# Performance work log

Measured on AMD Instinct MI355X. Metric: run time of the kernel, lower is better.

## Reference

```python
import jax, jax.numpy as jnp
import numpy as np

ALPHA = 0.05
GDEP = 2


def conv1x1(x, w, b):
    # x: [N,C,V,L], w: [O,C], b: [O]
    return jnp.einsum('ncvl,oc->novl', x, w) + b[None, :, None, None]


def setup_inputs() -> dict:
    key = jax.random.key(0)
    ks = jax.random.split(key, 9)
    N, C, V, L = 32, 32, 400, 12
    c_out = 32
    cat = (GDEP + 1) * C
    s = 0.05
    return {
        'x': jax.random.normal(ks[0], (N, C, V, L), jnp.float32),
        'w_lin1': jax.random.normal(ks[1], (C, C), jnp.float32) * s,
        'b_lin1': jnp.zeros((C,), jnp.float32),
        'w_lin2': jax.random.normal(ks[2], (C, C), jnp.float32) * s,
        'b_lin2': jnp.zeros((C,), jnp.float32),
        'w_mlp1': jax.random.normal(ks[3], (c_out, cat), jnp.float32) * s,
        'b_mlp1': jnp.zeros((c_out,), jnp.float32),
        'w_mlp2': jax.random.normal(ks[4], (c_out, cat), jnp.float32) * s,
        'b_mlp2': jnp.zeros((c_out,), jnp.float32),
    }


def reference(x, w_lin1, b_lin1, w_lin2, b_lin2, w_mlp1, b_mlp1, w_mlp2, b_mlp2):
    # dynamic adjacency: adj[n,v,w,l] = sum_c x1[n,c,v,l] * x2[n,c,w,l]
    x1 = jnp.tanh(conv1x1(x, w_lin1, b_lin1))
    x2 = jnp.tanh(conv1x1(x, w_lin2, b_lin2))
    adj = jnp.einsum('ncvl,ncwl->nvwl', x1, x2)  # [N,V,V,L]
    adj0 = jax.nn.softmax(adj, axis=2)
    adj1 = jax.nn.softmax(jnp.swapaxes(adj, 1, 2), axis=2)

    def diffuse(a):
        h = x
        out = [h]
        for _ in range(GDEP):
            # nconv: h[n,c,w,l] = sum_v h[n,c,v,l] * a[n,v,w,l]
            h = ALPHA * x + (1.0 - ALPHA) * jnp.einsum('ncvl,nvwl->ncwl', h, a)
            out.append(h)
        return jnp.concatenate(out, axis=1)  # [N,(GDEP+1)*C,V,L]

    ho1 = conv1x1(diffuse(adj0), w_mlp1, b_mlp1)
    ho2 = conv1x1(diffuse(adj1), w_mlp2, b_mlp2)
    return ho1 + ho2
```

## Files before the change

### kernel.cpp

```cpp
#include <hip/hip_runtime.h>
#include <stdint.h>

#define TT 1024
#define AL 0.05f
#define OM 0.95f
#define STRD 408
#define LOG2E 1.4426950408889634f

typedef short s4v __attribute__((ext_vector_type(4)));
typedef short s8v __attribute__((ext_vector_type(8)));
typedef float f4v __attribute__((ext_vector_type(4)));
typedef float f16v __attribute__((ext_vector_type(16)));
typedef int   i2v __attribute__((ext_vector_type(2)));

#define MF32(a,b,c) __builtin_amdgcn_mfma_f32_32x32x16_bf16(a,b,c,0,0,0)
#define MF16(a,b,c) __builtin_amdgcn_mfma_f32_16x16x32_bf16(a,b,c,0,0,0)
#define MFP32(a,b,c) __builtin_amdgcn_mfma_f32_32x32x16_fp8_fp8(a,b,c,0,0,0)
#define MFP16(a,b,c) __builtin_amdgcn_mfma_f32_16x16x32_fp8_fp8(a,b,c,0,0,0)

#if __has_builtin(__builtin_amdgcn_exp2f)
#define E2(x) __builtin_amdgcn_exp2f(x)
#else
#define E2(x) exp2f(x)
#endif

__device__ __forceinline__ uint16_t f2bf(float f){ union{float f;uint32_t i;}t; t.f=f; return (uint16_t)((t.i + 0x7fffu + ((t.i>>16)&1u))>>16); }
__device__ __forceinline__ float bf2f(uint16_t h){ union{uint32_t i;float f;}t; t.i=((uint32_t)h)<<16; return t.f; }
__device__ __forceinline__ float bfLO(uint32_t u){ union{uint32_t i;float f;}t; t.i=u<<16; return t.f; }
__device__ __forceinline__ float bfHI(uint32_t u){ union{uint32_t i;float f;}t; t.i=u&0xffff0000u; return t.f; }
__device__ __forceinline__ uint32_t cvtpk(float lo, float hi){ uint32_t r; asm("v_cvt_pk_bf16_f32 %0, %1, %2" : "=v"(r) : "v"(lo), "v"(hi)); return r; }
__device__ __forceinline__ void pl32swap(uint32_t &x, uint32_t &y){
#if __has_builtin(__builtin_amdgcn_permlane32_swap)
  i2v rr = __builtin_amdgcn_permlane32_swap((int)x, (int)y, false, false);
  x = (uint32_t)rr.x; y = (uint32_t)rr.y;
#else
  asm("v_permlane32_swap_b32 %0, %1" : "+v"(x), "+v"(y));
#endif
}
__device__ __forceinline__ float ftanh(float x){ float t = E2(2.885390081777927f*x); return __builtin_fmaf(-2.f, __builtin_amdgcn_rcpf(1.f + t), 1.f); }
__device__ __forceinline__ s8v ld8(const uint16_t* p){ return *(const s8v*)p; }

__device__ __forceinline__ uint32_t sw1fp8(float f){
  union{float f;uint32_t u;}t; t.f=f;
  uint32_t sgn=(t.u>>24)&0x80u; uint32_t a=t.u&0x7fffffffu;
  union{uint32_t u;float f;}af; af.u=a;
  if(af.f>448.f) return sgn|0x7eu;
  if(af.f<0.001953125f){ int q=(int)(af.f*512.f+0.5f); if(q>7)q=7; return sgn|(uint32_t)q; }
  uint32_t lsb=(a>>20)&1u; a+=0x0007ffffu+lsb;
  int ex=(int)(a>>23)-120; uint32_t man=(a>>20)&7u;
  if(ex>15||(ex==15&&man==7u)) return sgn|0x7eu;
  if(ex<=0){ int q=(int)(af.f*512.f+0.5f); if(q>7)q=7; return sgn|(uint32_t)q; }
  return sgn|((uint32_t)ex<<3)|man;
}
__device__ __forceinline__ uint32_t pk4fp8(float a,float b,float c,float d){
#if __has_builtin(__builtin_amdgcn_cvt_pk_fp8_f32)
  int v = __builtin_amdgcn_cvt_pk_fp8_f32(a,b,0,false);
  v = __builtin_amdgcn_cvt_pk_fp8_f32(c,d,v,true);
  return (uint32_t)v;
#else
  return sw1fp8(a) | (sw1fp8(b)<<8) | (sw1fp8(c)<<16) | (sw1fp8(d)<<24);
#endif
}
__device__ __forceinline__ s8v packw8(float4 f0, float4 f1){
  union{uint32_t d[4]; s8v v8;} A;
  A.d[0]=cvtpk(f0.x,f0.y); A.d[1]=cvtpk(f0.z,f0.w);
  A.d[2]=cvtpk(f1.x,f1.y); A.d[3]=cvtpk(f1.z,f1.w);
  return A.v8;
}

#define ROWF(e2) (((e2)&3) + 8*((e2)>>2) + 4*h2)
#define VXA(row,off) ((((row)<<5) + (off)) ^ (((row)&7)<<3))
#define VX8(row,b) ((((row)<<5) + (b)) ^ (((row)&3)<<4))

__device__ __align__(16) float gStage[32*12*12800];

#define X1B 0
#define X2B 12800
#define XCV 12800
#define GCV 25856
#define XTU 25856
#define RINV 38912
#define CINV 39312
#define HV 0
#define F2V 12800

__global__ __launch_bounds__(TT) void dymix(
    const float* __restrict__ x,
    const float* __restrict__ w1, const float* __restrict__ b1,
    const float* __restrict__ w2, const float* __restrict__ b2,
    const float* __restrict__ wm1, const float* __restrict__ bm1,
    const float* __restrict__ wm2, const float* __restrict__ bm2)
{
  __shared__ __align__(16) uint16_t S[39712];
  uint8_t* S8 = (uint8_t*)S;

  const int blk = blockIdx.x;
  const int xcd = blk & 7, slot = blk >> 3;
  const int n = xcd*4 + slot/12;
  const int l = slot - (slot/12)*12;
  const int t = threadIdx.x;
  const int wv = t >> 6;
  const int lane = t & 63;
  const int q  = lane >> 4;
  const int r  = lane & 15;
  const int h2 = lane >> 5;
  const int m32 = lane & 31;
  const long xbase = (long)n*153600 + l;

  for (int i = t; i < 12800; i += TT) {
    int c = i / 400, v = i - c*400;
    S[XCV + c*STRD + v] = f2bf(x[xbase + (long)i*12]);
  }
  __syncthreads();

  for (int i = t; i < 12800; i += TT) { int v = i>>5, c = i&31; S[XTU + VXA(v,c)] = S[XCV + c*STRD + v]; }
  __syncthreads();

  #pragma unroll
  for (int j = 0; j < 2; ++j) {
    int u = wv + 16*j;
    if (u < 24) {
      int nt = u >> 1, li = u & 1;
      const float* wsrc = li ? w2 : w1;
      const float* bsrc = li ? b2 : b1;
      uint8_t* dst8 = S8 + (li ? X2B : X1B);
      const float osc = li ? 1.f : LOG2E;
      f16v z = {};
      #pragma unroll
      for (int kk = 0; kk < 2; ++kk) {
        const float* wp = wsrc + m32*32 + kk*16 + h2*8;
        s8v a = packw8(*(const float4*)(wp), *(const float4*)(wp+4));
        s8v b = ld8(S + XTU + VXA(nt*32 + m32, kk*16 + h2*8));
        z = MF32(a, b, z);
      }
      int v = nt*32 + m32;
      #pragma unroll
      for (int g = 0; g < 4; ++g) {
        float4 bv = *(const float4*)(bsrc + 8*g + 4*h2);
        float p0 = ftanh(z[4*g+0] + bv.x) * osc;
        float p1 = ftanh(z[4*g+1] + bv.y) * osc;
        float p2 = ftanh(z[4*g+2] + bv.z) * osc;
        float p3 = ftanh(z[4*g+3] + bv.w) * osc;
        *(uint32_t*)(dst8 + VX8(v, 8*g + 4*h2)) = pk4fp8(p0,p1,p2,p3);
      }
    } else if (u < 28) {
      int li = (u-24)>>1, mt = u&1;
      const float* wsrc = li ? w2 : w1;
      const float* bsrc = li ? b2 : b1;
      uint8_t* dst8 = S8 + (li ? X2B : X1B);
      const float osc = li ? 1.f : LOG2E;
      const float* wp = wsrc + (mt*16 + r)*32 + q*8;
      s8v a = packw8(*(const float4*)(wp), *(const float4*)(wp+4));
      s8v b = ld8(S + XTU + VXA(384 + r, q*8));
      f4v z4 = {}; z4 = MF16(a, b, z4);
      float4 bv = *(const float4*)(bsrc + mt*16 + q*4);
      float p0 = ftanh(z4[0] + bv.x) * osc;
      float p1 = ftanh(z4[1] + bv.y) * osc;
      float p2 = ftanh(z4[2] + bv.z) * osc;
      float p3 = ftanh(z4[3] + bv.w) * osc;
      *(uint32_t*)(dst8 + VX8(384 + r, mt*16 + q*4)) = pk4fp8(p0,p1,p2,p3);
    }
  }
  s8v xf0, xf1, xft;
  {
    int m0 = (wv < 12) ? wv : 0;
    xf0 = ld8(S + XTU + VXA(m0*32 + m32, h2*8));
    xf1 = ld8(S + XTU + VXA(m0*32 + m32, 16 + h2*8));
    xft = ld8(S + XTU + VXA(384 + r, q*8));
  }
  __syncthreads();

  float* rsf = (float*)(S + GCV);
  float* csf = rsf + 400;
  for (int i = t; i < 400; i += TT) csf[i] = 0.f;
  __syncthreads();
  {
    long av8[2]; f4v rac[2] = {{},{}};
    #pragma unroll
    for (int jj = 0; jj < 2; ++jj) { int vt = wv + 16*jj; if (vt < 25) av8[jj] = *(const long*)(S8 + X1B + VX8(vt*16 + r, q*8)); }
    for (int wt = 0; wt < 25; ++wt) {
      long b8 = *(const long*)(S8 + X2B + VX8(wt*16 + r, q*8));
      float cp = 0.f;
      #pragma unroll
      for (int jj = 0; jj < 2; ++jj) {
        int vt = wv + 16*jj;
        if (vt < 25) {
          f4v z = {}; z = MFP16(av8[jj], b8, z);
          #pragma unroll
          for (int e = 0; e < 4; ++e) { float ev = E2(z[e]); rac[jj][e] += ev; cp += ev; }
        }
      }
      cp += __shfl_xor(cp, 16); cp += __shfl_xor(cp, 32);
      if (q == 0) atomicAdd(&csf[wt*16 + r], cp);
    }
    #pragma unroll
    for (int jj = 0; jj < 2; ++jj) {
      int vt = wv + 16*jj;
      if (vt < 25) {
        #pragma unroll
        for (int e = 0; e < 4; ++e) {
          float s = rac[jj][e];
          s += __shfl_xor(s,1); s += __shfl_xor(s,2); s += __shfl_xor(s,4); s += __shfl_xor(s,8);
          if (r == 0) rsf[vt*16 + q*4 + e] = s;
        }
      }
    }
  }
  __syncthreads();
  for (int i = t; i < 400; i += TT) { S[RINV + i] = f2bf(1.f/rsf[i]); S[CINV + i] = f2bf(1.f/csf[i]); }
  __syncthreads();

  f16v acc[2];
  for (int step = 0; step < 2; ++step) {
    { f16v zv = {}; acc[0]=zv; acc[1]=zv; }
    const uint16_t* AH = S + XCV;
    const uint16_t* AG = S + (step ? GCV : XCV);
    for (int sb = 0; sb < 13; ++sb) {
      const int vbase = sb*32;
      const bool lastsb = (sb == 12);
      const int kmax = lastsb ? 1 : 2;
      s8v fr[2][2];
      uint2 td0[2], td1[2];
      #pragma unroll
      for (int jj = 0; jj < 2; ++jj) {
        int g = wv + 16*jj;
        if (g >= 26) continue;
        int chain = (g < 13) ? 0 : 1;
        int uu = g - 13*chain;
        const uint8_t* sa8 = S8 + (chain ? X2B : X1B);
        const uint8_t* sb8 = S8 + (chain ? X1B : X2B);
        const int scl = chain ? CINV : RINV;
        if (uu < 12) {
          long a0 = *(const long*)(sa8 + VX8(vbase + m32, h2*8));
          long a1 = *(const long*)(sa8 + VX8(vbase + m32, 16 + h2*8));
          long b0 = *(const long*)(sb8 + VX8(uu*32 + m32, h2*8));
          long b1 = *(const long*)(sb8 + VX8(uu*32 + m32, 16 + h2*8));
          f16v z = {}; z = MFP32(a0, b0, z); z = MFP32(a1, b1, z);
          #pragma unroll
          for (int k = 0; k < 2; ++k) {
            if (k < kmax) {
              const uint16_t* spt = S + scl + vbase + 16*k + 4*h2;
              uint32_t sAB = *(const uint32_t*)(spt);
              uint32_t sCD = *(const uint32_t*)(spt + 2);
              uint32_t sEF = *(const uint32_t*)(spt + 8);
              uint32_t sGH = *(const uint32_t*)(spt + 10);
              uint32_t C0 = cvtpk(E2(z[8*k+0])*bfLO(sAB), E2(z[8*k+1])*bfHI(sAB));
              uint32_t C1 = cvtpk(E2(z[8*k+2])*bfLO(sCD), E2(z[8*k+3])*bfHI(sCD));
              uint32_t C2 = cvtpk(E2(z[8*k+4])*bfLO(sEF), E2(z[8*k+5])*bfHI(sEF));
              uint32_t C3 = cvtpk(E2(z[8*k+6])*bfLO(sGH), E2(z[8*k+7])*bfHI(sGH));
              pl32swap(C0, C2);
              pl32swap(C1, C3);
              union { uint32_t d[4]; s8v v8; } F;
              F.d[0] = C0; F.d[1] = C1; F.d[2] = C2; F.d[3] = C3;
              fr[jj][k] = F.v8;
            }
          }
        } else {
          long bT = *(const long*)(sb8 + VX8(384 + r, q*8));
          td1[jj].x = 0u; td1[jj].y = 0u;
          {
            long a = *(const long*)(sa8 + VX8(vbase + r, q*8));
            f4v z4 = {}; z4 = MFP16(a, bT, z4);
            float p0 = E2(z4[0]) * bf2f(S[scl + vbase + q*4 + 0]);
            float p1 = E2(z4[1]) * bf2f(S[scl + vbase + q*4 + 1]);
            float p2 = E2(z4[2]) * bf2f(S[scl + vbase + q*4 + 2]);
            float p3 = E2(z4[3]) * bf2f(S[scl + vbase + q*4 + 3]);
            td0[jj].x = cvtpk(p0,p1); td0[jj].y = cvtpk(p2,p3);
          }
          if (!lastsb) {
            long a = *(const long*)(sa8 + VX8(vbase + 16 + r, q*8));
            f4v z4 = {}; z4 = MFP16(a, bT, z4);
            float p0 = E2(z4[0]) * bf2f(S[scl + vbase + 16 + q*4 + 0]);
            float p1 = E2(z4[1]) * bf2f(S[scl + vbase + 16 + q*4 + 1]);
            float p2 = E2(z4[2]) * bf2f(S[scl + vbase + 16 + q*4 + 2]);
            float p3 = E2(z4[3]) * bf2f(S[scl + vbase + 16 + q*4 + 3]);
            td1[jj].x = cvtpk(p0,p1); td1[jj].y = cvtpk(p2,p3);
          }
        }
      }
      #pragma unroll
      for (int jj = 0; jj < 2; ++jj) {
        int g = wv + 16*jj;
        if (g >= 26) continue;
        int chain = (g < 13) ? 0 : 1;
        int uu = g - 13*chain;
        const uint16_t* Acv = chain ? AG : AH;
        if (uu < 12) {
          #pragma unroll
          for (int k = 0; k < 2; ++k) {
            if (k < kmax) {
              s8v a = ld8(Acv + m32*STRD + vbase + k*16 + h2*8);
              acc[jj] = MF32(a, fr[jj][k], acc[jj]);
            }
          }
        } else {
          const int src0 = (((q<<1)) & 3)*16 + r;
          const int src1 = (((q<<1)+1) & 3)*16 + r;
          uint32_t a0x = (uint32_t)__shfl((int)td0[jj].x, src0);
          uint32_t a0y = (uint32_t)__shfl((int)td0[jj].y, src0);
          uint32_t a1x = (uint32_t)__shfl((int)td1[jj].x, src0);
          uint32_t a1y = (uint32_t)__shfl((int)td1[jj].y, src0);
          uint32_t b0x = (uint32_t)__shfl((int)td0[jj].x, src1);
          uint32_t b0y = (uint32_t)__shfl((int)td0[jj].y, src1);
          uint32_t b1x = (uint32_t)__shfl((int)td1[jj].x, src1);
          uint32_t b1y = (uint32_t)__shfl((int)td1[jj].y, src1);
          const bool hi = (q >= 2);
          union { uint32_t u[4]; s8v v8; } B;
          B.u[0] = hi ? a1x : a0x;
          B.u[1] = hi ? a1y : a0y;
          B.u[2] = hi ? b1x : b0x;
          B.u[3] = hi ? b1y : b0y;
          #pragma unroll
          for (int mt2 = 0; mt2 < 2; ++mt2) {
            int koff = (lastsb && q >= 2) ? 0 : q*8;
            s8v a = ld8(Acv + (mt2*16 + r)*STRD + vbase + koff);
            f4v c4 = { acc[jj][4*mt2+0], acc[jj][4*mt2+1], acc[jj][4*mt2+2], acc[jj][4*mt2+3] };
            c4 = MF16(a, B.v8, c4);
            acc[jj][4*mt2+0]=c4[0]; acc[jj][4*mt2+1]=c4[1]; acc[jj][4*mt2+2]=c4[2]; acc[jj][4*mt2+3]=c4[3];
          }
        }
      }
    }
    __syncthreads();
    if (step == 0) {
      #pragma unroll
      for (int jj = 0; jj < 2; ++jj) {
        int g = wv + 16*jj;
        if (g >= 26) continue;
        int chain = (g < 13) ? 0 : 1;
        int uu = g - 13*chain;
        if (uu < 12) {
          int w = uu*32 + m32;
          #pragma unroll
          for (int e2 = 0; e2 < 16; ++e2) {
            int c = ROWF(e2);
            acc[jj][e2] = AL*bf2f(S[XCV + c*STRD + w]) + OM*acc[jj][e2];
          }
        } else {
          int w = 384 + r;
          #pragma unroll
          for (int mt2 = 0; mt2 < 2; ++mt2)
            #pragma unroll
            for (int e = 0; e < 4; ++e) {
              int c = mt2*16 + q*4 + e;
              acc[jj][4*mt2+e] = AL*bf2f(S[XCV + c*STRD + w]) + OM*acc[jj][4*mt2+e];
            }
        }
      }
      __syncthreads();
      #pragma unroll
      for (int jj = 0; jj < 2; ++jj) {
        int g = wv + 16*jj;
        if (g >= 26) continue;
        int chain = (g < 13) ? 0 : 1;
        int uu = g - 13*chain;
        uint16_t* dst = S + (chain ? GCV : XCV);
        if (uu < 12) {
          int w = uu*32 + m32;
          #pragma unroll
          for (int e2 = 0; e2 < 16; ++e2) { int c = ROWF(e2); dst[c*STRD + w] = f2bf(acc[jj][e2]); }
        } else {
          int w = 384 + r;
          #pragma unroll
          for (int mt2 = 0; mt2 < 2; ++mt2)
            #pragma unroll
            for (int e = 0; e < 4; ++e) { int c = mt2*16 + q*4 + e; dst[c*STRD + w] = f2bf(acc[jj][4*mt2+e]); }
        }
      }
      __syncthreads();
    }
  }

  for (int i = t; i < 12800; i += TT) { int v = i >> 5, c = i & 31; S[HV + VXA(v,c)] = S[XCV + c*STRD + v]; }
  __syncthreads();
  #pragma unroll
  for (int jj = 0; jj < 2; ++jj) {
    int g = wv + 16*jj;
    if (g >= 13) continue;
    int uu = g;
    uint16_t* dst = S + F2V;
    if (uu < 12) {
      int w = uu*32 + m32;
      #pragma unroll
      for (int gg = 0; gg < 4; ++gg) {
        uint2 d;
        d.x = cvtpk(OM*acc[jj][4*gg+0], OM*acc[jj][4*gg+1]);
        d.y = cvtpk(OM*acc[jj][4*gg+2], OM*acc[jj][4*gg+3]);
        *(uint2*)(dst + VXA(w, 8*gg + 4*h2)) = d;
      }
    } else {
      int w = 384 + r;
      #pragma unroll
      for (int mt2 = 0; mt2 < 2; ++mt2) {
        uint2 d;
        d.x = cvtpk(OM*acc[jj][4*mt2+0], OM*acc[jj][4*mt2+1]);
        d.y = cvtpk(OM*acc[jj][4*mt2+2], OM*acc[jj][4*mt2+3]);
        *(uint2*)(dst + VXA(w, mt2*16 + q*4)) = d;
      }
    }
  }
  __syncthreads();

  float* oSl = gStage + (long)(n*12 + l)*12800;
  {
    int m = wv;
    if (m < 12) {
      f16v z = {};
      #pragma unroll
      for (int p = 0; p < 3; ++p) {
        #pragma unroll
        for (int kk = 0; kk < 2; ++kk) {
          const float* wp = wm1 + m32*96 + p*32 + kk*16 + h2*8;
          float4 f0 = *(const float4*)(wp), f1 = *(const float4*)(wp+4);
          if (p == 0) {
            const float* wp2 = wm1 + m32*96 + 64 + kk*16 + h2*8;
            float4 g0 = *(const float4*)(wp2), g1 = *(const float4*)(wp2+4);
            f0.x += AL*g0.x; f0.y += AL*g0.y; f0.z += AL*g0.z; f0.w += AL*g0.w;
            f1.x += AL*g1.x; f1.y += AL*g1.y; f1.z += AL*g1.z; f1.w += AL*g1.w;
          }
          s8v a = packw8(f0, f1);
          s8v b = (p == 0) ? (kk ? xf1 : xf0)
                           : ld8(S + (p == 1 ? HV : F2V) + VXA(m*32 + m32, kk*16 + h2*8));
          z = MF32(a, b, z);
        }
      }
      int v = m*32 + m32;
      #pragma unroll
      for (int e2 = 0; e2 < 16; ++e2) { int o = ROWF(e2); oSl[o*400 + v] = z[e2] + bm1[o] + bm2[o]; }
    } else if (m < 14) {
      int mt = m - 12;
      f4v z4 = {};
      #pragma unroll
      for (int p = 0; p < 3; ++p) {
        const float* wp = wm1 + (mt*16 + r)*96 + p*32 + q*8;
        float4 f0 = *(const float4*)(wp), f1 = *(const float4*)(wp+4);
        if (p == 0) {
          const float* wp2 = wm1 + (mt*16 + r)*96 + 64 + q*8;
          float4 g0 = *(const float4*)(wp2), g1 = *(const float4*)(wp2+4);
          f0.x += AL*g0.x; f0.y += AL*g0.y; f0.z += AL*g0.z; f0.w += AL*g0.w;
          f1.x += AL*g1.x; f1.y += AL*g1.y; f1.z += AL*g1.z; f1.w += AL*g1.w;
        }
        s8v a = packw8(f0, f1);
        s8v b = (p == 0) ? xft : ld8(S + (p == 1 ? HV : F2V) + VXA(384 + r, q*8));
        z4 = MF16(a, b, z4);
      }
      #pragma unroll
      for (int e = 0; e < 4; ++e) { int o = mt*16 + q*4 + e; oSl[o*400 + 384 + r] = z4[e] + bm1[o] + bm2[o]; }
    }
  }
  __syncthreads();
  for (int i = t; i < 12800; i += TT) { int v = i >> 5, c = i & 31; S[HV + VXA(v,c)] = S[GCV + c*STRD + v]; }
  #pragma unroll
  for (int jj = 0; jj < 2; ++jj) {
    int g = wv + 16*jj;
    if (g < 13 || g >= 26) continue;
    int uu = g - 13;
    uint16_t* dst = S + F2V;
    if (uu < 12) {
      int w = uu*32 + m32;
      #pragma unroll
      for (int gg = 0; gg < 4; ++gg) {
        uint2 d;
        d.x = cvtpk(OM*acc[jj][4*gg+0], OM*acc[jj][4*gg+1]);
        d.y = cvtpk(OM*acc[jj][4*gg+2], OM*acc[jj][4*gg+3]);
        *(uint2*)(dst + VXA(w, 8*gg + 4*h2)) = d;
      }
    } else {
      int w = 384 + r;
      #pragma unroll
      for (int mt2 = 0; mt2 < 2; ++mt2) {
        uint2 d;
        d.x = cvtpk(OM*acc[jj][4*mt2+0], OM*acc[jj][4*mt2+1]);
        d.y = cvtpk(OM*acc[jj][4*mt2+2], OM*acc[jj][4*mt2+3]);
        *(uint2*)(dst + VXA(w, mt2*16 + q*4)) = d;
      }
    }
  }
  __syncthreads();
  {
    int m = wv;
    if (m < 12) {
      f16v z = {};
      #pragma unroll
      for (int p = 0; p < 3; ++p) {
        #pragma unroll
        for (int kk = 0; kk < 2; ++kk) {
          const float* wp = wm2 + m32*96 + p*32 + kk*16 + h2*8;
          float4 f0 = *(const float4*)(wp), f1 = *(const float4*)(wp+4);
          if (p == 0) {
            const float* wp2 = wm2 + m32*96 + 64 + kk*16 + h2*8;
            float4 g0 = *(const float4*)(wp2), g1 = *(const float4*)(wp2+4);
            f0.x += AL*g0.x; f0.y += AL*g0.y; f0.z += AL*g0.z; f0.w += AL*g0.w;
            f1.x += AL*g1.x; f1.y += AL*g1.y; f1.z += AL*g1.z; f1.w += AL*g1.w;
          }
          s8v a = packw8(f0, f1);
          s8v b = (p == 0) ? (kk ? xf1 : xf0)
                           : ld8(S + (p == 1 ? HV : F2V) + VXA(m*32 + m32, kk*16 + h2*8));
          z = MF32(a, b, z);
        }
      }
      int v = m*32 + m32;
      #pragma unroll
      for (int e2 = 0; e2 < 16; ++e2) { int o = ROWF(e2); oSl[o*400 + v] += z[e2]; }
    } else if (m < 14) {
      int mt = m - 12;
      f4v z4 = {};
      #pragma unroll
      for (int p = 0; p < 3; ++p) {
        const float* wp = wm2 + (mt*16 + r)*96 + p*32 + q*8;
        float4 f0 = *(const float4*)(wp), f1 = *(const float4*)(wp+4);
        if (p == 0) {
          const float* wp2 = wm2 + (mt*16 + r)*96 + 64 + q*8;
          float4 g0 = *(const float4*)(wp2), g1 = *(const float4*)(wp2+4);
          f0.x += AL*g0.x; f0.y += AL*g0.y; f0.z += AL*g0.z; f0.w += AL*g0.w;
          f1.x += AL*g1.x; f1.y += AL*g1.y; f1.z += AL*g1.z; f1.w += AL*g1.w;
        }
        s8v a = packw8(f0, f1);
        s8v b = (p == 0) ? xft : ld8(S + (p == 1 ? HV : F2V) + VXA(384 + r, q*8));
        z4 = MF16(a, b, z4);
      }
      #pragma unroll
      for (int e = 0; e < 4; ++e) { int o = mt*16 + q*4 + e; oSl[o*400 + 384 + r] += z4[e]; }
    }
  }
}

__global__ __launch_bounds__(256) void finT(float* __restrict__ out) {
  int idx = blockIdx.x*256 + threadIdx.x;
  int n = idx / 12800, ov = idx - n*12800;
  const float* src = gStage + (long)n*153600 + ov;
  float vals[12];
  #pragma unroll
  for (int l = 0; l < 12; ++l) vals[l] = src[(long)l*12800];
  float4* dst = (float4*)(out + (long)idx*12);
  dst[0] = make_float4(vals[0],vals[1],vals[2],vals[3]);
  dst[1] = make_float4(vals[4],vals[5],vals[6],vals[7]);
  dst[2] = make_float4(vals[8],vals[9],vals[10],vals[11]);
}

extern "C" void kernel_launch(void* const* d_in, const int* in_sizes, int n_in,
                              void* d_out, int out_size, void* d_ws, size_t ws_size,
                              hipStream_t stream) {
  (void)in_sizes; (void)n_in; (void)out_size; (void)d_ws; (void)ws_size;
  dymix<<<dim3(384), dim3(TT), 0, stream>>>(
      (const float*)d_in[0],
      (const float*)d_in[1], (const float*)d_in[2],
      (const float*)d_in[3], (const float*)d_in[4],
      (const float*)d_in[5], (const float*)d_in[6],
      (const float*)d_in[7], (const float*)d_in[8]);
  finT<<<dim3(1600), dim3(256), 0, stream>>>((float*)d_out);
}
```

Measured before the change: 254.2 us.

## Halve block size to 512 threads with four work items per wave

Cuts the block from 1024 to 512 threads (8 waves) and gives each wave twice the work items in every phase: projection, row and column sums, diffusion, and output MLPs. The diffusion loop also fuses the softmax-fragment build with its MFMA accumulation, so fragment arrays are no longer held across a second loop. The aim is more per-wave ILP and a launch-bounds hint, at the cost of higher register pressure from four accumulators per wave and fewer waves to hide latency. LDS use per block is unchanged, so block residency per CU may not change.

```diff
diff --git a/kernel.cpp b/kernel.cpp
--- a/kernel.cpp
+++ b/kernel.cpp
@@ -1,7 +1,7 @@
 #include <hip/hip_runtime.h>
 #include <stdint.h>
 
-#define TT 1024
+#define TT 512
 #define AL 0.05f
 #define OM 0.95f
 #define STRD 408
@@ -84,7 +84,7 @@
 #define HV 0
 #define F2V 12800
 
-__global__ __launch_bounds__(TT) void dymix(
+__global__ __launch_bounds__(TT, 4) void dymix(
     const float* __restrict__ x,
     const float* __restrict__ w1, const float* __restrict__ b1,
     const float* __restrict__ w2, const float* __restrict__ b2,
@@ -117,8 +117,8 @@
   __syncthreads();
 
   #pragma unroll
-  for (int j = 0; j < 2; ++j) {
-    int u = wv + 16*j;
+  for (int j = 0; j < 4; ++j) {
+    int u = wv + 8*j;
     if (u < 24) {
       int nt = u >> 1, li = u & 1;
       const float* wsrc = li ? w2 : w1;
@@ -161,12 +161,14 @@
       *(uint32_t*)(dst8 + VX8(384 + r, mt*16 + q*4)) = pk4fp8(p0,p1,p2,p3);
     }
   }
-  s8v xf0, xf1, xft;
+  s8v xf0a, xf1a, xf0b, xf1b, xft;
   {
-    int m0 = (wv < 12) ? wv : 0;
-    xf0 = ld8(S + XTU + VXA(m0*32 + m32, h2*8));
-    xf1 = ld8(S + XTU + VXA(m0*32 + m32, 16 + h2*8));
-    xft = ld8(S + XTU + VXA(384 + r, q*8));
+    xf0a = ld8(S + XTU + VXA(wv*32 + m32, h2*8));
+    xf1a = ld8(S + XTU + VXA(wv*32 + m32, 16 + h2*8));
+    int mb = (wv < 4) ? (wv + 8) : 0;
+    xf0b = ld8(S + XTU + VXA(mb*32 + m32, h2*8));
+    xf1b = ld8(S + XTU + VXA(mb*32 + m32, 16 + h2*8));
+    xft  = ld8(S + XTU + VXA(384 + r, q*8));
   }
   __syncthreads();
 
@@ -175,15 +177,15 @@
   for (int i = t; i < 400; i += TT) csf[i] = 0.f;
   __syncthreads();
   {
-    long av8[2]; f4v rac[2] = {{},{}};
+    long av8[4]; f4v rac[4] = {{},{},{},{}};
     #pragma unroll
-    for (int jj = 0; jj < 2; ++jj) { int vt = wv + 16*jj; if (vt < 25) av8[jj] = *(const long*)(S8 + X1B + VX8(vt*16 + r, q*8)); }
+    for (int jj = 0; jj < 4; ++jj) { int vt = wv + 8*jj; if (vt < 25) av8[jj] = *(const long*)(S8 + X1B + VX8(vt*16 + r, q*8)); }
     for (int wt = 0; wt < 25; ++wt) {
       long b8 = *(const long*)(S8 + X2B + VX8(wt*16 + r, q*8));
       float cp = 0.f;
       #pragma unroll
-      for (int jj = 0; jj < 2; ++jj) {
-        int vt = wv + 16*jj;
+      for (int jj = 0; jj < 4; ++jj) {
+        int vt = wv + 8*jj;
         if (vt < 25) {
           f4v z = {}; z = MFP16(av8[jj], b8, z);
           #pragma unroll
@@ -194,8 +196,8 @@
       if (q == 0) atomicAdd(&csf[wt*16 + r], cp);
     }
     #pragma unroll
-    for (int jj = 0; jj < 2; ++jj) {
-      int vt = wv + 16*jj;
+    for (int jj = 0; jj < 4; ++jj) {
+      int vt = wv + 8*jj;
       if (vt < 25) {
         #pragma unroll
         for (int e = 0; e < 4; ++e) {
@@ -210,26 +212,25 @@
   for (int i = t; i < 400; i += TT) { S[RINV + i] = f2bf(1.f/rsf[i]); S[CINV + i] = f2bf(1.f/csf[i]); }
   __syncthreads();
 
-  f16v acc[2];
+  f16v acc[4];
   for (int step = 0; step < 2; ++step) {
-    { f16v zv = {}; acc[0]=zv; acc[1]=zv; }
+    { f16v zv = {}; acc[0]=zv; acc[1]=zv; acc[2]=zv; acc[3]=zv; }
     const uint16_t* AH = S + XCV;
     const uint16_t* AG = S + (step ? GCV : XCV);
     for (int sb = 0; sb < 13; ++sb) {
       const int vbase = sb*32;
       const bool lastsb = (sb == 12);
       const int kmax = lastsb ? 1 : 2;
-      s8v fr[2][2];
-      uint2 td0[2], td1[2];
-      #pragma unroll
-      for (int jj = 0; jj < 2; ++jj) {
-        int g = wv + 16*jj;
+      #pragma unroll
+      for (int jj = 0; jj < 4; ++jj) {
+        int g = wv + 8*jj;
         if (g >= 26) continue;
         int chain = (g < 13) ? 0 : 1;
         int uu = g - 13*chain;
         const uint8_t* sa8 = S8 + (chain ? X2B : X1B);
         const uint8_t* sb8 = S8 + (chain ? X1B : X2B);
         const int scl = chain ? CINV : RINV;
+        const uint16_t* Acv = chain ? AG : AH;
         if (uu < 12) {
           long a0 = *(const long*)(sa8 + VX8(vbase + m32, h2*8));
           long a1 = *(const long*)(sa8 + VX8(vbase + m32, 16 + h2*8));
@@ -252,12 +253,13 @@
               pl32swap(C1, C3);
               union { uint32_t d[4]; s8v v8; } F;
               F.d[0] = C0; F.d[1] = C1; F.d[2] = C2; F.d[3] = C3;
-              fr[jj][k] = F.v8;
+              s8v a = ld8(Acv + m32*STRD + vbase + k*16 + h2*8);
+              acc[jj] = MF32(a, F.v8, acc[jj]);
             }
           }
         } else {
           long bT = *(const long*)(sb8 + VX8(384 + r, q*8));
-          td1[jj].x = 0u; td1[jj].y = 0u;
+          uint2 td0, td1; td1.x = 0u; td1.y = 0u;
           {
             long a = *(const long*)(sa8 + VX8(vbase + r, q*8));
             f4v z4 = {}; z4 = MFP16(a, bT, z4);
@@ -265,7 +267,7 @@
             float p1 = E2(z4[1]) * bf2f(S[scl + vbase + q*4 + 1]);
             float p2 = E2(z4[2]) * bf2f(S[scl + vbase + q*4 + 2]);
             float p3 = E2(z4[3]) * bf2f(S[scl + vbase + q*4 + 3]);
-            td0[jj].x = cvtpk(p0,p1); td0[jj].y = cvtpk(p2,p3);
+            td0.x = cvtpk(p0,p1); td0.y = cvtpk(p2,p3);
           }
           if (!lastsb) {
             long a = *(const long*)(sa8 + VX8(vbase + 16 + r, q*8));
@@ -274,36 +276,18 @@
             float p1 = E2(z4[1]) * bf2f(S[scl + vbase + 16 + q*4 + 1]);
             float p2 = E2(z4[2]) * bf2f(S[scl + vbase + 16 + q*4 + 2]);
             float p3 = E2(z4[3]) * bf2f(S[scl + vbase + 16 + q*4 + 3]);
-            td1[jj].x = cvtpk(p0,p1); td1[jj].y = cvtpk(p2,p3);
-          }
-        }
-      }
-      #pragma unroll
-      for (int jj = 0; jj < 2; ++jj) {
-        int g = wv + 16*jj;
-        if (g >= 26) continue;
-        int chain = (g < 13) ? 0 : 1;
-        int uu = g - 13*chain;
-        const uint16_t* Acv = chain ? AG : AH;
-        if (uu < 12) {
-          #pragma unroll
-          for (int k = 0; k < 2; ++k) {
-            if (k < kmax) {
-              s8v a = ld8(Acv + m32*STRD + vbase + k*16 + h2*8);
-              acc[jj] = MF32(a, fr[jj][k], acc[jj]);
-            }
-          }
-        } else {
+            td1.x = cvtpk(p0,p1); td1.y = cvtpk(p2,p3);
+          }
           const int src0 = (((q<<1)) & 3)*16 + r;
           const int src1 = (((q<<1)+1) & 3)*16 + r;
-          uint32_t a0x = (uint32_t)__shfl((int)td0[jj].x, src0);
-          uint32_t a0y = (uint32_t)__shfl((int)td0[jj].y, src0);
-          uint32_t a1x = (uint32_t)__shfl((int)td1[jj].x, src0);
-          uint32_t a1y = (uint32_t)__shfl((int)td1[jj].y, src0);
-          uint32_t b0x = (uint32_t)__shfl((int)td0[jj].x, src1);
-          uint32_t b0y = (uint32_t)__shfl((int)td0[jj].y, src1);
-          uint32_t b1x = (uint32_t)__shfl((int)td1[jj].x, src1);
-          uint32_t b1y = (uint32_t)__shfl((int)td1[jj].y, src1);
+          uint32_t a0x = (uint32_t)__shfl((int)td0.x, src0);
+          uint32_t a0y = (uint32_t)__shfl((int)td0.y, src0);
+          uint32_t a1x = (uint32_t)__shfl((int)td1.x, src0);
+          uint32_t a1y = (uint32_t)__shfl((int)td1.y, src0);
+          uint32_t b0x = (uint32_t)__shfl((int)td0.x, src1);
+          uint32_t b0y = (uint32_t)__shfl((int)td0.y, src1);
+          uint32_t b1x = (uint32_t)__shfl((int)td1.x, src1);
+          uint32_t b1y = (uint32_t)__shfl((int)td1.y, src1);
           const bool hi = (q >= 2);
           union { uint32_t u[4]; s8v v8; } B;
           B.u[0] = hi ? a1x : a0x;
@@ -324,8 +308,8 @@
     __syncthreads();
     if (step == 0) {
       #pragma unroll
-      for (int jj = 0; jj < 2; ++jj) {
-        int g = wv + 16*jj;
+      for (int jj = 0; jj < 4; ++jj) {
+        int g = wv + 8*jj;
         if (g >= 26) continue;
         int chain = (g < 13) ? 0 : 1;
         int uu = g - 13*chain;
@@ -349,8 +333,8 @@
       }
       __syncthreads();
       #pragma unroll
-      for (int jj = 0; jj < 2; ++jj) {
-        int g = wv + 16*jj;
+      for (int jj = 0; jj < 4; ++jj) {
+        int g = wv + 8*jj;
         if (g >= 26) continue;
         int chain = (g < 13) ? 0 : 1;
         int uu = g - 13*chain;
@@ -374,8 +358,8 @@
   for (int i = t; i < 12800; i += TT) { int v = i >> 5, c = i & 31; S[HV + VXA(v,c)] = S[XCV + c*STRD + v]; }
   __syncthreads();
   #pragma unroll
-  for (int jj = 0; jj < 2; ++jj) {
-    int g = wv + 16*jj;
+  for (int jj = 0; jj < 4; ++jj) {
+    int g = wv + 8*jj;
     if (g >= 13) continue;
     int uu = g;
     uint16_t* dst = S + F2V;
@@ -402,8 +386,9 @@
   __syncthreads();
 
   float* oSl = gStage + (long)(n*12 + l)*12800;
-  {
-    int m = wv;
+  #pragma unroll
+  for (int jm = 0; jm < 2; ++jm) {
+    int m = wv + 8*jm;
     if (m < 12) {
       f16v z = {};
       #pragma unroll
@@ -419,8 +404,9 @@
             f1.x += AL*g1.x; f1.y += AL*g1.y; f1.z += AL*g1.z; f1.w += AL*g1.w;
           }
           s8v a = packw8(f0, f1);
-          s8v b = (p == 0) ? (kk ? xf1 : xf0)
-                           : ld8(S + (p == 1 ? HV : F2V) + VXA(m*32 + m32, kk*16 + h2*8));
+          s8v b;
+          if (p == 0) b = jm ? (kk ? xf1b : xf0b) : (kk ? xf1a : xf0a);
+          else        b = ld8(S + (p == 1 ? HV : F2V) + VXA(m*32 + m32, kk*16 + h2*8));
           z = MF32(a, b, z);
         }
       }
@@ -451,8 +437,8 @@
   __syncthreads();
   for (int i = t; i < 12800; i += TT) { int v = i >> 5, c = i & 31; S[HV + VXA(v,c)] = S[GCV + c*STRD + v]; }
   #pragma unroll
-  for (int jj = 0; jj < 2; ++jj) {
-    int g = wv + 16*jj;
+  for (int jj = 0; jj < 4; ++jj) {
+    int g = wv + 8*jj;
     if (g < 13 || g >= 26) continue;
     int uu = g - 13;
     uint16_t* dst = S + F2V;
@@ -477,8 +463,9 @@
     }
   }
   __syncthreads();
-  {
-    int m = wv;
+  #pragma unroll
+  for (int jm = 0; jm < 2; ++jm) {
+    int m = wv + 8*jm;
     if (m < 12) {
       f16v z = {};
       #pragma unroll
@@ -494,8 +481,9 @@
             f1.x += AL*g1.x; f1.y += AL*g1.y; f1.z += AL*g1.z; f1.w += AL*g1.w;
           }
           s8v a = packw8(f0, f1);
-          s8v b = (p == 0) ? (kk ? xf1 : xf0)
-                           : ld8(S + (p == 1 ? HV : F2V) + VXA(m*32 + m32, kk*16 + h2*8));
+          s8v b;
+          if (p == 0) b = jm ? (kk ? xf1b : xf0b) : (kk ? xf1a : xf0a);
+          else        b = ld8(S + (p == 1 ? HV : F2V) + VXA(m*32 + m32, kk*16 + h2*8));
           z = MF32(a, b, z);
         }
       }
```

After: 219.1 us. 1.16x faster.
